# Kernel optimization log

Measured on AMD Instinct MI355X. Metric: run time of the kernel, lower is better.

Reference implementation:

```python
import jax, jax.numpy as jnp
import numpy as np
import math

HIDDEN = 4096
N_HEADS = 32
HEAD_DIM = HIDDEN // N_HEADS
MAX_POS = 4096
BASE = 10000.0
NEG_INF = jnp.finfo(jnp.float32).min


def rotate_half(x):
    x1, x2 = jnp.split(x, 2, axis=-1)
    return jnp.concatenate((-x2, x1), axis=-1)


def rope_tables(seq_len, dtype=jnp.float32):
    inv_freq = 1.0 / (BASE ** (jnp.arange(0, HEAD_DIM, 2, dtype=jnp.float32) / HEAD_DIM))
    t = jnp.arange(seq_len, dtype=jnp.float32)
    freqs = jnp.einsum('i,j->ij', t, inv_freq)  # [S, D/2]
    emb = jnp.concatenate((freqs, freqs), axis=-1)  # [S, D]
    return jnp.cos(emb).astype(dtype), jnp.sin(emb).astype(dtype)


def setup_inputs() -> dict:
    key = jax.random.key(0)
    k1, k2, k3 = jax.random.split(key, 3)
    bsz, q_len = 2, 2048
    hidden_states = jax.random.normal(k1, (bsz, q_len, HIDDEN), dtype=jnp.float32)
    # causal additive mask [bsz, 1, q, q]: 0 on/below diag, large-negative above
    causal = jnp.triu(jnp.full((q_len, q_len), NEG_INF, dtype=jnp.float32), k=1)
    attention_mask = jnp.broadcast_to(causal[None, None], (bsz, 1, q_len, q_len))
    position_ids = jnp.broadcast_to(jnp.arange(q_len, dtype=jnp.int64)[None], (bsz, q_len))
    W_pack = jax.random.normal(k2, (3 * HIDDEN, HIDDEN), dtype=jnp.float32) * (1.0 / math.sqrt(HIDDEN))
    W_o = jax.random.normal(k3, (HIDDEN, HIDDEN), dtype=jnp.float32) * (1.0 / math.sqrt(HIDDEN))
    return {"hidden_states": hidden_states, "attention_mask": attention_mask,
            "position_ids": position_ids, "W_pack": W_pack, "W_o": W_o}


def reference(hidden_states, attention_mask, position_ids, W_pack, W_o):
    bsz, q_len, _ = hidden_states.shape
    proj = jnp.einsum('bsh,oh->bso', hidden_states, W_pack)  # [B,S,3H]
    q, k, v = jnp.split(proj, 3, axis=-1)
    def shape(x):
        return x.reshape(bsz, q_len, N_HEADS, HEAD_DIM).transpose(0, 2, 1, 3)  # [B,nH,S,D]
    q, k, v = shape(q), shape(k), shape(v)
    cos, sin = rope_tables(q_len, hidden_states.dtype)
    cos = cos[position_ids][:, None]  # [B,1,S,D]
    sin = sin[position_ids][:, None]
    q = q * cos + rotate_half(q) * sin
    k = k * cos + rotate_half(k) * sin
    scores = jnp.einsum('bhqd,bhkd->bhqk', q, k) / math.sqrt(HEAD_DIM)
    scores = scores + attention_mask
    scores = jnp.maximum(scores, NEG_INF)
    w = jax.nn.softmax(scores.astype(jnp.float32), axis=-1).astype(q.dtype)
    out = jnp.einsum('bhqk,bhkd->bhqd', w, v)
    out = out.transpose(0, 2, 1, 3).reshape(bsz, q_len, HIDDEN)
    return jnp.einsum('bsh,oh->bso', out, W_o)
```

## Files before the change

### kernel.cpp

```cpp
#include <hip/hip_runtime.h>
#include <hip/hip_bf16.h>

typedef __bf16 bf16x8 __attribute__((ext_vector_type(8)));
typedef float f32x4 __attribute__((ext_vector_type(4)));

#define HIDDEN 4096
#define NH 32
#define HD 128
#define SEQ 2048
#define BATCH 2
#define MTOT 4096
#define QKV 12288

__device__ __forceinline__ void async16(const void* g, void* l) {
    __builtin_amdgcn_global_load_lds(
        (const __attribute__((address_space(1))) void*)(uintptr_t)g,
        (__attribute__((address_space(3))) void*)(uint32_t)(uintptr_t)l,
        16, 0, 0);
}

__device__ __forceinline__ uint4 ld8(const __hip_bfloat16* p) { return *(const uint4*)p; }
__device__ __forceinline__ uint4 ld8(const float* p) {
    float4 a = *(const float4*)p;
    float4 b = *(const float4*)(p + 4);
    __hip_bfloat16 t[8];
    t[0] = __float2bfloat16(a.x); t[1] = __float2bfloat16(a.y);
    t[2] = __float2bfloat16(a.z); t[3] = __float2bfloat16(a.w);
    t[4] = __float2bfloat16(b.x); t[5] = __float2bfloat16(b.y);
    t[6] = __float2bfloat16(b.z); t[7] = __float2bfloat16(b.w);
    return *(uint4*)t;
}

__device__ __forceinline__ void stc(__hip_bfloat16* C, size_t i, float v) { C[i] = __float2bfloat16(v); }
__device__ __forceinline__ void stc(float* C, size_t i, float v) { C[i] = v; }

__global__ __launch_bounds__(256) void cvt_bf16(const float* __restrict__ src,
                                                __hip_bfloat16* __restrict__ dst, int n8) {
    int i = blockIdx.x * 256 + threadIdx.x;
    if (i < n8) *(uint4*)&dst[(size_t)i * 8] = ld8(&src[(size_t)i * 8]);
}

template <typename TC>
__global__ __launch_bounds__(512) void gemm_256(const __hip_bfloat16* __restrict__ A,
                                                const __hip_bfloat16* __restrict__ Bt,
                                                TC* __restrict__ C,
                                                int M, int N, int K, int lda) {
    __shared__ __align__(16) __hip_bfloat16 As[4][256][32];
    __shared__ __align__(16) __hip_bfloat16 Bs[4][256][32];
    const int bn = blockIdx.x * 256, bm = blockIdx.y * 256;
    const int tid = threadIdx.x, wave = tid >> 6, lane = tid & 63;
    const int wm = wave >> 2, wn = wave & 3;
    const int row16 = lane & 15, quad = lane >> 4;
    const int lr = lane >> 2;
    const int lc = (lane & 3) * 8;
    const __hip_bfloat16* Ab = A + (size_t)(bm + wave * 16 + lr) * lda + lc;
    const __hip_bfloat16* Bb = Bt + (size_t)(bn + wave * 16 + lr) * K + lc;
    const int NT = K >> 5;

    f32x4 acc[8][4] = {};

    auto stage = [&](int t) {
        const int s = t & 3;
        const int kt = t << 5;
        async16(Ab + kt,                     &As[s][wave * 16][0]);
        async16(Ab + (size_t)128 * lda + kt, &As[s][wave * 16 + 128][0]);
        async16(Bb + kt,                     &Bs[s][wave * 16][0]);
        async16(Bb + (size_t)128 * K + kt,   &Bs[s][wave * 16 + 128][0]);
    };

    stage(0); stage(1); stage(2);

    for (int t = 0; t < NT; ++t) {
        const int s = t & 3;
        const int rem = NT - 1 - t;
        if (rem >= 2)      asm volatile("s_waitcnt vmcnt(8)" ::: "memory");
        else if (rem == 1) asm volatile("s_waitcnt vmcnt(4)" ::: "memory");
        else               asm volatile("s_waitcnt vmcnt(0)" ::: "memory");
        __builtin_amdgcn_s_barrier();
        __builtin_amdgcn_sched_barrier(0);
        if (t + 3 < NT) stage(t + 3);
        bf16x8 af[8], bf[4];
#pragma unroll
        for (int i = 0; i < 8; ++i)
            af[i] = *(const bf16x8*)&As[s][wm * 128 + i * 16 + row16][quad * 8];
#pragma unroll
        for (int j = 0; j < 4; ++j)
            bf[j] = *(const bf16x8*)&Bs[s][wn * 64 + j * 16 + row16][quad * 8];
        __builtin_amdgcn_s_setprio(1);
#pragma unroll
        for (int i = 0; i < 8; ++i)
#pragma unroll
            for (int j = 0; j < 4; ++j)
                acc[i][j] = __builtin_amdgcn_mfma_f32_16x16x32_bf16(af[i], bf[j], acc[i][j], 0, 0, 0);
        __builtin_amdgcn_s_setprio(0);
    }

    const int col0 = bn + wn * 64 + row16;
    const int row0 = bm + wm * 128 + quad * 4;
#pragma unroll
    for (int i = 0; i < 8; ++i)
#pragma unroll
        for (int j = 0; j < 4; ++j)
#pragma unroll
            for (int rg = 0; rg < 4; ++rg)
                stc(C, (size_t)(row0 + i * 16 + rg) * N + col0 + j * 16, acc[i][j][rg]);
}

template <typename TA, typename TB, typename TC>
__global__ __launch_bounds__(256) void gemm_bt(const TA* __restrict__ A,
                                               const TB* __restrict__ Bt,
                                               TC* __restrict__ C,
                                               int M, int N, int K, int lda) {
    __shared__ __align__(16) __hip_bfloat16 As[128][32];
    __shared__ __align__(16) __hip_bfloat16 Bs[128][32];
    const int bn = blockIdx.x * 128, bm = blockIdx.y * 128;
    const int tid = threadIdx.x, wave = tid >> 6, lane = tid & 63;
    const int wm = (wave >> 1) * 64, wn = (wave & 1) * 64;
    const int row16 = lane & 15, quad = lane >> 4;
    const int arow = tid >> 2;
    const int acol = (tid & 3) * 8;

    f32x4 acc[4][4] = {};

    for (int kt = 0; kt < K; kt += 32) {
        __syncthreads();
#pragma unroll
        for (int it = 0; it < 2; ++it) {
            int r = arow + it * 64;
            *(uint4*)&As[r][acol] = ld8(&A[(size_t)(bm + r) * lda + kt + acol]);
            *(uint4*)&Bs[r][acol] = ld8(&Bt[(size_t)(bn + r) * K + kt + acol]);
        }
        __syncthreads();
        bf16x8 af[4], bf[4];
#pragma unroll
        for (int i = 0; i < 4; ++i) af[i] = *(const bf16x8*)&As[wm + i * 16 + row16][quad * 8];
#pragma unroll
        for (int j = 0; j < 4; ++j) bf[j] = *(const bf16x8*)&Bs[wn + j * 16 + row16][quad * 8];
#pragma unroll
        for (int i = 0; i < 4; ++i)
#pragma unroll
            for (int j = 0; j < 4; ++j)
                acc[i][j] = __builtin_amdgcn_mfma_f32_16x16x32_bf16(af[i], bf[j], acc[i][j], 0, 0, 0);
    }
    const int col0 = bn + wn + row16;
    const int row0 = bm + wm + quad * 4;
#pragma unroll
    for (int i = 0; i < 4; ++i)
#pragma unroll
        for (int j = 0; j < 4; ++j)
#pragma unroll
            for (int rg = 0; rg < 4; ++rg)
                stc(C, (size_t)(row0 + i * 16 + rg) * N + col0 + j * 16, acc[i][j][rg]);
}

__global__ __launch_bounds__(256) void rope_kernel(__hip_bfloat16* __restrict__ proj) {
    int t = blockIdx.x * 256 + threadIdx.x;
    int j = t & 63;
    int head = (t >> 6) & 31;
    int mat = (t >> 11) & 1;
    int row = t >> 12;
    int pos = row & (SEQ - 1);
    float invf = __expf(-(float)j * 0.14391156514261f);
    float ang = (float)pos * invf;
    float rev = ang * 0.15915494309189535f;
    rev -= floorf(rev);
    float arad = rev * 6.283185307179586f;
    float sn = __sinf(arad);
    float cs = __cosf(arad);
    if (mat == 0) {
        sn *= 0.08838834764831845f;
        cs *= 0.08838834764831845f;
    }
    size_t base = (size_t)row * QKV + mat * HIDDEN + head * HD + j;
    float x1 = __bfloat162float(proj[base]);
    float x2 = __bfloat162float(proj[base + 64]);
    proj[base]      = __float2bfloat16(x1 * cs - x2 * sn);
    proj[base + 64] = __float2bfloat16(x2 * cs + x1 * sn);
}

__global__ __launch_bounds__(256) void transpose_v(const __hip_bfloat16* __restrict__ proj,
                                                   __hip_bfloat16* __restrict__ vtg) {
    __shared__ __hip_bfloat16 Ls[64][132];
    const int st = blockIdx.x, bh = blockIdx.y;
    const int b = bh >> 5, h = bh & 31;
    const int s0 = st << 6;
    const int tid = threadIdx.x;
    const __hip_bfloat16* vb = proj + (size_t)b * SEQ * QKV + 2 * HIDDEN + h * HD;
    for (int i = tid; i < 1024; i += 256) {
        int r = i >> 4, c = (i & 15) << 3;
        uint4 raw = *(const uint4*)&vb[(size_t)(s0 + r) * QKV + c];
        *(uint2*)&Ls[r][c]     = make_uint2(raw.x, raw.y);
        *(uint2*)&Ls[r][c + 4] = make_uint2(raw.z, raw.w);
    }
    __syncthreads();
    __hip_bfloat16* ob = vtg + (size_t)bh * HD * SEQ + s0;
    for (int t = tid; t < 1024; t += 256) {
        int d = t >> 3, sc = (t & 7) << 3;
        __hip_bfloat16 tmp[8];
#pragma unroll
        for (int x = 0; x < 8; ++x) tmp[x] = Ls[sc + x][d];
        *(uint4*)&ob[(size_t)d * SEQ + sc] = *(uint4*)tmp;
    }
}

__global__ __launch_bounds__(256) void attn_mfma(__hip_bfloat16* __restrict__ proj,
                                                 const __hip_bfloat16* __restrict__ vtg) {
    __shared__ __align__(16) __hip_bfloat16 Ks[64][136];
    __shared__ __align__(16) __hip_bfloat16 Vs[128][72];
    __shared__ __align__(16) __hip_bfloat16 Ps[4][32][72];
    const int nwg = gridDim.x * gridDim.y;
    const int f  = blockIdx.y * gridDim.x + blockIdx.x;
    const int f2 = (f & 7) * (nwg >> 3) + (f >> 3);
    const int qt = f2 & 15;
    const int bh = f2 >> 4;
    const int b = bh >> 5, h = bh & 31;
    const int q0 = qt << 7;
    const int tid = threadIdx.x, wave = tid >> 6, lane = tid & 63;
    const int row16 = lane & 15, quad = lane >> 4;

    __hip_bfloat16* qb = proj + (size_t)b * SEQ * QKV + h * HD;
    const __hip_bfloat16* kb = qb + HIDDEN;
    const __hip_bfloat16* vp = vtg + (size_t)bh * HD * SEQ;

    const int wbase = q0 + wave * 32;

    bf16x8 qf[2][4];
#pragma unroll
    for (int qr = 0; qr < 2; ++qr) {
        const __hip_bfloat16* qrow = qb + (size_t)(wbase + qr * 16 + row16) * QKV + quad * 8;
#pragma unroll
        for (int s = 0; s < 4; ++s) qf[qr][s] = *(const bf16x8*)(qrow + s * 32);
    }

    f32x4 oa[2][8] = {};
    float m_i[2][4], l_i[2][4];
#pragma unroll
    for (int qr = 0; qr < 2; ++qr)
#pragma unroll
        for (int r = 0; r < 4; ++r) { m_i[qr][r] = -3.0e38f; l_i[qr][r] = 0.f; }

    const int ktmax = 2 * qt + 1;
    for (int kt = 0; kt <= ktmax; ++kt) {
        const int k0 = kt << 6;
        __syncthreads();
        for (int i = tid; i < 1024; i += 256) {
            int r = i >> 4, c = (i & 15) << 3;
            *(uint4*)&Ks[r][c] = *(const uint4*)&kb[(size_t)(k0 + r) * QKV + c];
        }
        for (int i = tid; i < 1024; i += 256) {
            int d = i >> 3, ko = (i & 7) << 3;
            *(uint4*)&Vs[d][ko] = *(const uint4*)&vp[(size_t)d * SEQ + k0 + ko];
        }
        __syncthreads();
        if (k0 > wbase + 31) continue;

        f32x4 sf[2][4] = {};
#pragma unroll
        for (int nt = 0; nt < 4; ++nt) {
            bf16x8 kf[4];
#pragma unroll
            for (int ks = 0; ks < 4; ++ks)
                kf[ks] = *(const bf16x8*)&Ks[nt * 16 + row16][ks * 32 + quad * 8];
#pragma unroll
            for (int qr = 0; qr < 2; ++qr)
#pragma unroll
                for (int ks = 0; ks < 4; ++ks)
                    sf[qr][nt] = __builtin_amdgcn_mfma_f32_16x16x32_bf16(qf[qr][ks], kf[ks], sf[qr][nt], 0, 0, 0);
        }
        if (k0 + 63 > wbase) {
#pragma unroll
            for (int qr = 0; qr < 2; ++qr)
#pragma unroll
                for (int nt = 0; nt < 4; ++nt) {
                    int key = k0 + nt * 16 + row16;
#pragma unroll
                    for (int rg = 0; rg < 4; ++rg)
                        if (key > wbase + qr * 16 + quad * 4 + rg) sf[qr][nt][rg] = -3.0e38f;
                }
        }
#pragma unroll
        for (int qr = 0; qr < 2; ++qr) {
            float alpha[4], rs[4];
#pragma unroll
            for (int rg = 0; rg < 4; ++rg) {
                float mx = fmaxf(fmaxf(sf[qr][0][rg], sf[qr][1][rg]), fmaxf(sf[qr][2][rg], sf[qr][3][rg]));
#pragma unroll
                for (int off = 8; off > 0; off >>= 1) mx = fmaxf(mx, __shfl_xor(mx, off));
                float mn = fmaxf(m_i[qr][rg], mx);
                alpha[rg] = __expf(m_i[qr][rg] - mn);
                m_i[qr][rg] = mn;
                rs[rg] = 0.f;
            }
#pragma unroll
            for (int nt = 0; nt < 4; ++nt)
#pragma unroll
                for (int rg = 0; rg < 4; ++rg) {
                    float p = __expf(sf[qr][nt][rg] - m_i[qr][rg]);
                    rs[rg] += p;
                    Ps[wave][qr * 16 + quad * 4 + rg][nt * 16 + row16] = __float2bfloat16(p);
                }
#pragma unroll
            for (int rg = 0; rg < 4; ++rg) {
#pragma unroll
                for (int off = 8; off > 0; off >>= 1) rs[rg] += __shfl_xor(rs[rg], off);
                l_i[qr][rg] = l_i[qr][rg] * alpha[rg] + rs[rg];
            }
#pragma unroll
            for (int dt = 0; dt < 8; ++dt)
#pragma unroll
                for (int rg = 0; rg < 4; ++rg) oa[qr][dt][rg] *= alpha[rg];
        }
        __builtin_amdgcn_wave_barrier();
        bf16x8 pf[2][2];
#pragma unroll
        for (int qr = 0; qr < 2; ++qr) {
            pf[qr][0] = *(const bf16x8*)&Ps[wave][qr * 16 + row16][quad * 8];
            pf[qr][1] = *(const bf16x8*)&Ps[wave][qr * 16 + row16][32 + quad * 8];
        }
#pragma unroll
        for (int dt = 0; dt < 8; ++dt) {
            bf16x8 v0 = *(const bf16x8*)&Vs[dt * 16 + row16][quad * 8];
            bf16x8 v1 = *(const bf16x8*)&Vs[dt * 16 + row16][32 + quad * 8];
#pragma unroll
            for (int qr = 0; qr < 2; ++qr) {
                oa[qr][dt] = __builtin_amdgcn_mfma_f32_16x16x32_bf16(pf[qr][0], v0, oa[qr][dt], 0, 0, 0);
                oa[qr][dt] = __builtin_amdgcn_mfma_f32_16x16x32_bf16(pf[qr][1], v1, oa[qr][dt], 0, 0, 0);
            }
        }
    }
#pragma unroll
    for (int qr = 0; qr < 2; ++qr)
#pragma unroll
        for (int rg = 0; rg < 4; ++rg) {
            float inv = 1.0f / l_i[qr][rg];
            __hip_bfloat16* orow = qb + (size_t)(wbase + qr * 16 + quad * 4 + rg) * QKV;
#pragma unroll
            for (int dt = 0; dt < 8; ++dt)
                orow[dt * 16 + row16] = __float2bfloat16(oa[qr][dt][rg] * inv);
        }
}

extern "C" void kernel_launch(void* const* d_in, const int* in_sizes, int n_in,
                              void* d_out, int out_size, void* d_ws, size_t ws_size,
                              hipStream_t stream) {
    const float* hs = (const float*)d_in[0];
    const float* Wp = (const float*)d_in[3];
    const float* Wo = (const float*)d_in[4];
    float* out = (float*)d_out;

    const size_t SZ_PROJ = (size_t)MTOT * QKV;
    const size_t SZ_H    = (size_t)MTOT * HIDDEN;
    const size_t SZ_WP   = (size_t)QKV * HIDDEN;
    const size_t need = (SZ_PROJ + SZ_H + SZ_WP + SZ_H) * sizeof(__hip_bfloat16);

    __hip_bfloat16* proj = (__hip_bfloat16*)d_ws;

    if (ws_size >= need) {
        __hip_bfloat16* hsb = proj + SZ_PROJ;
        __hip_bfloat16* Wpb = hsb + SZ_H;
        __hip_bfloat16* Wob = Wpb + SZ_WP;
        __hip_bfloat16* vtg = hsb;

        cvt_bf16<<<dim3(SZ_H / 8 / 256), dim3(256), 0, stream>>>(hs, hsb, SZ_H / 8);
        cvt_bf16<<<dim3(SZ_WP / 8 / 256), dim3(256), 0, stream>>>(Wp, Wpb, SZ_WP / 8);
        cvt_bf16<<<dim3(SZ_H / 8 / 256), dim3(256), 0, stream>>>(Wo, Wob, SZ_H / 8);
        gemm_256<<<dim3(QKV / 256, MTOT / 256), dim3(512), 0, stream>>>(hsb, Wpb, proj, MTOT, QKV, HIDDEN, HIDDEN);
        rope_kernel<<<dim3((MTOT * 2 * NH * 64) / 256), dim3(256), 0, stream>>>(proj);
        transpose_v<<<dim3(SEQ / 64, BATCH * NH), dim3(256), 0, stream>>>(proj, vtg);
        attn_mfma<<<dim3(SEQ / 128, BATCH * NH), dim3(256), 0, stream>>>(proj, vtg);
        gemm_256<<<dim3(HIDDEN / 256, MTOT / 256), dim3(512), 0, stream>>>(proj, Wob, out, MTOT, HIDDEN, HIDDEN, QKV);
    } else {
        __hip_bfloat16* vtg = proj + SZ_PROJ;
        gemm_bt<<<dim3(QKV / 128, MTOT / 128), dim3(256), 0, stream>>>(hs, Wp, proj, MTOT, QKV, HIDDEN, HIDDEN);
        rope_kernel<<<dim3((MTOT * 2 * NH * 64) / 256), dim3(256), 0, stream>>>(proj);
        transpose_v<<<dim3(SEQ / 64, BATCH * NH), dim3(256), 0, stream>>>(proj, vtg);
        attn_mfma<<<dim3(SEQ / 128, BATCH * NH), dim3(256), 0, stream>>>(proj, vtg);
        gemm_bt<<<dim3(HIDDEN / 128, MTOT / 128), dim3(256), 0, stream>>>(proj, Wo, out, MTOT, HIDDEN, HIDDEN, QKV);
    }
}
```

Measured before the change: 1.246 ms.

## Double-buffer K/V tiles with async LDS loads and widen attention blocks

The attention kernel now uses 8 waves per block covering 256 query rows, loads K and V tiles straight into LDS with global_load_lds into a double buffer laid out in MFMA fragment order, and prefetches the next tile while computing the current one. This aims to hide global load latency and halve K/V traffic per query row through more reuse. In exchange the grid has half as many blocks, causal work per block is more imbalanced, and each block uses more LDS.

```diff
diff --git a/kernel.cpp b/kernel.cpp
--- a/kernel.cpp
+++ b/kernel.cpp
@@ -203,18 +203,18 @@
     }
 }
 
-__global__ __launch_bounds__(256) void attn_mfma(__hip_bfloat16* __restrict__ proj,
+__global__ __launch_bounds__(512) void attn_mfma(__hip_bfloat16* __restrict__ proj,
                                                  const __hip_bfloat16* __restrict__ vtg) {
-    __shared__ __align__(16) __hip_bfloat16 Ks[64][136];
-    __shared__ __align__(16) __hip_bfloat16 Vs[128][72];
-    __shared__ __align__(16) __hip_bfloat16 Ps[4][32][72];
+    __shared__ __align__(16) __hip_bfloat16 Kf[2][16][512];
+    __shared__ __align__(16) __hip_bfloat16 Vf[2][16][512];
+    __shared__ __align__(16) __hip_bfloat16 Ps[8][32][72];
     const int nwg = gridDim.x * gridDim.y;
     const int f  = blockIdx.y * gridDim.x + blockIdx.x;
     const int f2 = (f & 7) * (nwg >> 3) + (f >> 3);
-    const int qt = f2 & 15;
-    const int bh = f2 >> 4;
+    const int qt = f2 & 7;
+    const int bh = f2 >> 3;
     const int b = bh >> 5, h = bh & 31;
-    const int q0 = qt << 7;
+    const int q0 = qt << 8;
     const int tid = threadIdx.x, wave = tid >> 6, lane = tid & 63;
     const int row16 = lane & 15, quad = lane >> 4;
 
@@ -224,6 +224,21 @@
 
     const int wbase = q0 + wave * 32;
 
+    const int b0 = 2 * wave, b1 = 2 * wave + 1;
+    const __hip_bfloat16* ks0 = kb + (size_t)((b0 >> 2) * 16 + row16) * QKV + (b0 & 3) * 32 + quad * 8;
+    const __hip_bfloat16* ks1 = kb + (size_t)((b1 >> 2) * 16 + row16) * QKV + (b1 & 3) * 32 + quad * 8;
+    const __hip_bfloat16* vs0 = vp + (size_t)((b0 >> 1) * 16 + row16) * SEQ + (b0 & 1) * 32 + quad * 8;
+    const __hip_bfloat16* vs1 = vp + (size_t)((b1 >> 1) * 16 + row16) * SEQ + (b1 & 1) * 32 + quad * 8;
+
+    auto stage = [&](int kt) {
+        const int s = kt & 1;
+        const int k0 = kt << 6;
+        async16(ks0 + (size_t)k0 * QKV, &Kf[s][b0][0]);
+        async16(ks1 + (size_t)k0 * QKV, &Kf[s][b1][0]);
+        async16(vs0 + k0,               &Vf[s][b0][0]);
+        async16(vs1 + k0,               &Vf[s][b1][0]);
+    };
+
     bf16x8 qf[2][4];
 #pragma unroll
     for (int qr = 0; qr < 2; ++qr) {
@@ -239,94 +254,94 @@
 #pragma unroll
         for (int r = 0; r < 4; ++r) { m_i[qr][r] = -3.0e38f; l_i[qr][r] = 0.f; }
 
-    const int ktmax = 2 * qt + 1;
+    stage(0);
+    asm volatile("s_waitcnt vmcnt(0)" ::: "memory");
+    __builtin_amdgcn_s_barrier();
+    __builtin_amdgcn_sched_barrier(0);
+
+    const int ktmax = 4 * qt + 3;
     for (int kt = 0; kt <= ktmax; ++kt) {
+        const int s = kt & 1;
         const int k0 = kt << 6;
-        __syncthreads();
-        for (int i = tid; i < 1024; i += 256) {
-            int r = i >> 4, c = (i & 15) << 3;
-            *(uint4*)&Ks[r][c] = *(const uint4*)&kb[(size_t)(k0 + r) * QKV + c];
+        if (kt < ktmax) stage(kt + 1);
+        if (k0 <= wbase + 31) {
+            f32x4 sf[2][4] = {};
+#pragma unroll
+            for (int nt = 0; nt < 4; ++nt) {
+                bf16x8 kf[4];
+#pragma unroll
+                for (int ks = 0; ks < 4; ++ks)
+                    kf[ks] = *(const bf16x8*)&Kf[s][nt * 4 + ks][lane * 8];
+#pragma unroll
+                for (int qr = 0; qr < 2; ++qr)
+#pragma unroll
+                    for (int ks = 0; ks < 4; ++ks)
+                        sf[qr][nt] = __builtin_amdgcn_mfma_f32_16x16x32_bf16(qf[qr][ks], kf[ks], sf[qr][nt], 0, 0, 0);
+            }
+            if (k0 + 63 > wbase) {
+#pragma unroll
+                for (int qr = 0; qr < 2; ++qr)
+#pragma unroll
+                    for (int nt = 0; nt < 4; ++nt) {
+                        int key = k0 + nt * 16 + row16;
+#pragma unroll
+                        for (int rg = 0; rg < 4; ++rg)
+                            if (key > wbase + qr * 16 + quad * 4 + rg) sf[qr][nt][rg] = -3.0e38f;
+                    }
+            }
+#pragma unroll
+            for (int qr = 0; qr < 2; ++qr) {
+                float alpha[4], rs[4];
+#pragma unroll
+                for (int rg = 0; rg < 4; ++rg) {
+                    float mx = fmaxf(fmaxf(sf[qr][0][rg], sf[qr][1][rg]), fmaxf(sf[qr][2][rg], sf[qr][3][rg]));
+#pragma unroll
+                    for (int off = 8; off > 0; off >>= 1) mx = fmaxf(mx, __shfl_xor(mx, off));
+                    float mn = fmaxf(m_i[qr][rg], mx);
+                    alpha[rg] = __expf(m_i[qr][rg] - mn);
+                    m_i[qr][rg] = mn;
+                    rs[rg] = 0.f;
+                }
+#pragma unroll
+                for (int nt = 0; nt < 4; ++nt)
+#pragma unroll
+                    for (int rg = 0; rg < 4; ++rg) {
+                        float p = __expf(sf[qr][nt][rg] - m_i[qr][rg]);
+                        rs[rg] += p;
+                        Ps[wave][qr * 16 + quad * 4 + rg][nt * 16 + row16] = __float2bfloat16(p);
+                    }
+#pragma unroll
+                for (int rg = 0; rg < 4; ++rg) {
+#pragma unroll
+                    for (int off = 8; off > 0; off >>= 1) rs[rg] += __shfl_xor(rs[rg], off);
+                    l_i[qr][rg] = l_i[qr][rg] * alpha[rg] + rs[rg];
+                }
+#pragma unroll
+                for (int dt = 0; dt < 8; ++dt)
+#pragma unroll
+                    for (int rg = 0; rg < 4; ++rg) oa[qr][dt][rg] *= alpha[rg];
+            }
+            __builtin_amdgcn_wave_barrier();
+            bf16x8 pf[2][2];
+#pragma unroll
+            for (int qr = 0; qr < 2; ++qr) {
+                pf[qr][0] = *(const bf16x8*)&Ps[wave][qr * 16 + row16][quad * 8];
+                pf[qr][1] = *(const bf16x8*)&Ps[wave][qr * 16 + row16][32 + quad * 8];
+            }
+#pragma unroll
+            for (int dt = 0; dt < 8; ++dt) {
+                bf16x8 v0 = *(const bf16x8*)&Vf[s][dt * 2][lane * 8];
+                bf16x8 v1 = *(const bf16x8*)&Vf[s][dt * 2 + 1][lane * 8];
+#pragma unroll
+                for (int qr = 0; qr < 2; ++qr) {
+                    oa[qr][dt] = __builtin_amdgcn_mfma_f32_16x16x32_bf16(pf[qr][0], v0, oa[qr][dt], 0, 0, 0);
+                    oa[qr][dt] = __builtin_amdgcn_mfma_f32_16x16x32_bf16(pf[qr][1], v1, oa[qr][dt], 0, 0, 0);
+                }
+            }
         }
-        for (int i = tid; i < 1024; i += 256) {
-            int d = i >> 3, ko = (i & 7) << 3;
-            *(uint4*)&Vs[d][ko] = *(const uint4*)&vp[(size_t)d * SEQ + k0 + ko];
-        }
-        __syncthreads();
-        if (k0 > wbase + 31) continue;
-
-        f32x4 sf[2][4] = {};
-#pragma unroll
-        for (int nt = 0; nt < 4; ++nt) {
-            bf16x8 kf[4];
-#pragma unroll
-            for (int ks = 0; ks < 4; ++ks)
-                kf[ks] = *(const bf16x8*)&Ks[nt * 16 + row16][ks * 32 + quad * 8];
-#pragma unroll
-            for (int qr = 0; qr < 2; ++qr)
-#pragma unroll
-                for (int ks = 0; ks < 4; ++ks)
-                    sf[qr][nt] = __builtin_amdgcn_mfma_f32_16x16x32_bf16(qf[qr][ks], kf[ks], sf[qr][nt], 0, 0, 0);
-        }
-        if (k0 + 63 > wbase) {
-#pragma unroll
-            for (int qr = 0; qr < 2; ++qr)
-#pragma unroll
-                for (int nt = 0; nt < 4; ++nt) {
-                    int key = k0 + nt * 16 + row16;
-#pragma unroll
-                    for (int rg = 0; rg < 4; ++rg)
-                        if (key > wbase + qr * 16 + quad * 4 + rg) sf[qr][nt][rg] = -3.0e38f;
-                }
-        }
-#pragma unroll
-        for (int qr = 0; qr < 2; ++qr) {
-            float alpha[4], rs[4];
-#pragma unroll
-            for (int rg = 0; rg < 4; ++rg) {
-                float mx = fmaxf(fmaxf(sf[qr][0][rg], sf[qr][1][rg]), fmaxf(sf[qr][2][rg], sf[qr][3][rg]));
-#pragma unroll
-                for (int off = 8; off > 0; off >>= 1) mx = fmaxf(mx, __shfl_xor(mx, off));
-                float mn = fmaxf(m_i[qr][rg], mx);
-                alpha[rg] = __expf(m_i[qr][rg] - mn);
-                m_i[qr][rg] = mn;
-                rs[rg] = 0.f;
-            }
-#pragma unroll
-            for (int nt = 0; nt < 4; ++nt)
-#pragma unroll
-                for (int rg = 0; rg < 4; ++rg) {
-                    float p = __expf(sf[qr][nt][rg] - m_i[qr][rg]);
-                    rs[rg] += p;
-                    Ps[wave][qr * 16 + quad * 4 + rg][nt * 16 + row16] = __float2bfloat16(p);
-                }
-#pragma unroll
-            for (int rg = 0; rg < 4; ++rg) {
-#pragma unroll
-                for (int off = 8; off > 0; off >>= 1) rs[rg] += __shfl_xor(rs[rg], off);
-                l_i[qr][rg] = l_i[qr][rg] * alpha[rg] + rs[rg];
-            }
-#pragma unroll
-            for (int dt = 0; dt < 8; ++dt)
-#pragma unroll
-                for (int rg = 0; rg < 4; ++rg) oa[qr][dt][rg] *= alpha[rg];
-        }
-        __builtin_amdgcn_wave_barrier();
-        bf16x8 pf[2][2];
-#pragma unroll
-        for (int qr = 0; qr < 2; ++qr) {
-            pf[qr][0] = *(const bf16x8*)&Ps[wave][qr * 16 + row16][quad * 8];
-            pf[qr][1] = *(const bf16x8*)&Ps[wave][qr * 16 + row16][32 + quad * 8];
-        }
-#pragma unroll
-        for (int dt = 0; dt < 8; ++dt) {
-            bf16x8 v0 = *(const bf16x8*)&Vs[dt * 16 + row16][quad * 8];
-            bf16x8 v1 = *(const bf16x8*)&Vs[dt * 16 + row16][32 + quad * 8];
-#pragma unroll
-            for (int qr = 0; qr < 2; ++qr) {
-                oa[qr][dt] = __builtin_amdgcn_mfma_f32_16x16x32_bf16(pf[qr][0], v0, oa[qr][dt], 0, 0, 0);
-                oa[qr][dt] = __builtin_amdgcn_mfma_f32_16x16x32_bf16(pf[qr][1], v1, oa[qr][dt], 0, 0, 0);
-            }
-        }
+        asm volatile("s_waitcnt vmcnt(0)" ::: "memory");
+        __builtin_amdgcn_s_barrier();
+        __builtin_amdgcn_sched_barrier(0);
     }
 #pragma unroll
     for (int qr = 0; qr < 2; ++qr)
@@ -367,14 +382,14 @@
         gemm_256<<<dim3(QKV / 256, MTOT / 256), dim3(512), 0, stream>>>(hsb, Wpb, proj, MTOT, QKV, HIDDEN, HIDDEN);
         rope_kernel<<<dim3((MTOT * 2 * NH * 64) / 256), dim3(256), 0, stream>>>(proj);
         transpose_v<<<dim3(SEQ / 64, BATCH * NH), dim3(256), 0, stream>>>(proj, vtg);
-        attn_mfma<<<dim3(SEQ / 128, BATCH * NH), dim3(256), 0, stream>>>(proj, vtg);
+        attn_mfma<<<dim3(SEQ / 256, BATCH * NH), dim3(512), 0, stream>>>(proj, vtg);
         gemm_256<<<dim3(HIDDEN / 256, MTOT / 256), dim3(512), 0, stream>>>(proj, Wob, out, MTOT, HIDDEN, HIDDEN, QKV);
     } else {
         __hip_bfloat16* vtg = proj + SZ_PROJ;
         gemm_bt<<<dim3(QKV / 128, MTOT / 128), dim3(256), 0, stream>>>(hs, Wp, proj, MTOT, QKV, HIDDEN, HIDDEN);
         rope_kernel<<<dim3((MTOT * 2 * NH * 64) / 256), dim3(256), 0, stream>>>(proj);
         transpose_v<<<dim3(SEQ / 64, BATCH * NH), dim3(256), 0, stream>>>(proj, vtg);
-        attn_mfma<<<dim3(SEQ / 128, BATCH * NH), dim3(256), 0, stream>>>(proj, vtg);
+        attn_mfma<<<dim3(SEQ / 256, BATCH * NH), dim3(512), 0, stream>>>(proj, vtg);
         gemm_bt<<<dim3(HIDDEN / 128, MTOT / 128), dim3(256), 0, stream>>>(proj, Wo, out, MTOT, HIDDEN, HIDDEN, QKV);
     }
 }
```

After: 1.199 ms. 1.04x faster.
